# Kernel optimization log

Measured on AMD Instinct MI355X. Metric: run time of the kernel, lower is better.

Reference implementation:

```python
import jax, jax.numpy as jnp
import numpy as np

B = 131072
E = 116            # embedding dim; 12 + E = 128 = layer_sizes[0]
H = 256            # MLP hidden
LATENT = 64

PAIRS = [(0, 1), (0, 2), (1, 2)]
IDS = np.array([[0, 3, 4], [1, 5, 6], [2, 7, 8]])  # ids_in_config, indexed by pair count


def setup_inputs() -> dict:
    key = jax.random.key(0)
    ks = jax.random.split(key, 12)
    d_in = 12 + E  # 128
    s = lambda k, shape, fan_in: jax.random.normal(k, shape, jnp.float32) / np.sqrt(fan_in)
    return {
        "initial_s": jax.random.normal(ks[0], (B, 9), jnp.float32),
        "current_s": jax.random.normal(ks[1], (B, 9), jnp.float32),
        "embeddings": jax.random.normal(ks[2], (B, E), jnp.float32),
        "W1": s(ks[3], (d_in, H), d_in),
        "b1": jnp.zeros((H,), jnp.float32),
        "W2": s(ks[4], (H, H), H),
        "b2": jnp.zeros((H,), jnp.float32),
        "Wm": s(ks[5], (H, LATENT), H),
        "bm": jnp.zeros((LATENT,), jnp.float32),
        "Wv": s(ks[6], (H, LATENT), H),
        "bv": jnp.zeros((LATENT,), jnp.float32),
    }


def _build_inp(initial_s, current_s, embeddings):
    # Replicates the pairwise one-hot + gather + concat construction.
    bsz = initial_s.shape[0]
    eye = jnp.eye(3, dtype=initial_s.dtype)
    feats = []
    for c, (i, j) in enumerate(PAIRS):
        oh = jnp.broadcast_to(jnp.concatenate([eye[i], eye[j]]), (bsz, 6))
        idx = IDS[c]
        feats.append(jnp.concatenate(
            [oh, initial_s[:, idx], current_s[:, idx], embeddings], axis=-1))
    return jnp.stack(feats)  # (3, B, 12+E)


def reference(initial_s, current_s, embeddings, W1, b1, W2, b2, Wm, bm, Wv, bv):
    inp = _build_inp(initial_s, current_s, embeddings)      # (3, B, 128)
    x = jax.nn.relu(jnp.einsum('pbi,ih->pbh', inp, W1) + b1)  # (3, B, 256)
    x = jax.nn.relu(jnp.einsum('pbh,hk->pbk', x, W2) + b2)    # (3, B, 256)
    means = jnp.einsum('pbh,hl->pbl', x, Wm) + bm             # (3, B, 64)
    log_vars = jnp.einsum('pbh,hl->pbl', x, Wv) + bv          # (3, B, 64)
    return (means, log_vars)
```

## Files before the change

kernel.cpp:

```cpp
#include <hip/hip_runtime.h>

typedef __attribute__((ext_vector_type(8))) __bf16 bf16x8;
typedef __attribute__((ext_vector_type(4))) float f32x4;
typedef unsigned int u32;
typedef unsigned long long u64;
typedef unsigned short u16;

#define NB 131072
#define TPB 8

__device__ __forceinline__ u16 f2bf(float f) {
  unsigned int u = __builtin_bit_cast(unsigned int, f);
  u += 0x7fffu + ((u >> 16) & 1u);
  return (u16)(u >> 16);
}

__device__ __forceinline__ u32 cvt_pk(float lo, float hi) {
  u32 r;
  asm("v_cvt_pk_bf16_f32 %0, %1, %2" : "=v"(r) : "v"(lo), "v"(hi));
  return r;
}

#define INP_ADDR(r, byte) (((r) << 8) + ((byte) ^ (((r) & 7) << 4)))
#define X_ADDR(r, byte)   (((r) << 9) + ((byte) ^ (((r) & 7) << 4)))

__global__ void prep_kernel(const float* __restrict__ W1, const float* __restrict__ b1,
                            const float* __restrict__ W2,
                            const float* __restrict__ Wm, const float* __restrict__ Wv,
                            u16* __restrict__ W1f, u16* __restrict__ W2f,
                            u16* __restrict__ Whf, float* __restrict__ b1p) {
  int tid = blockIdx.x * 256 + threadIdx.x;
  int NT = gridDim.x * 256;
  for (int i = tid; i < 32768; i += NT) {
    int j = i & 7, lane = (i >> 3) & 63, f = i >> 9;
    int nf = f & 15, kf = f >> 4;
    int n = nf * 16 + (lane & 15);
    int k = kf * 32 + 8 * (lane >> 4) + j;
    W1f[i] = f2bf(W1[k * 256 + n]);
  }
  for (int i = tid; i < 65536; i += NT) {
    int j = i & 7, lane = (i >> 3) & 63, f = i >> 9;
    int nf = f & 15, kf = f >> 4;
    int n = nf * 16 + (lane & 15);
    int k = kf * 32 + 8 * (lane >> 4) + j;
    W2f[i] = f2bf(W2[k * 256 + n]);
  }
  for (int i = tid; i < 32768; i += NT) {
    int j = i & 7, lane = (i >> 3) & 63, f = i >> 9;
    int nf = f & 7, kf = f >> 3;
    int n = nf * 16 + (lane & 15);
    int k = kf * 32 + 8 * (lane >> 4) + j;
    Whf[i] = f2bf(n < 64 ? Wm[k * 64 + n] : Wv[k * 64 + (n - 64)]);
  }
  if (tid < 768) {
    int p = tid >> 8, h = tid & 255;
    const int r1[3] = {0, 0, 1};
    const int r2[3] = {4, 5, 5};
    b1p[tid] = b1[h] + W1[r1[p] * 256 + h] + W1[r2[p] * 256 + h];
  }
}

__global__ __launch_bounds__(512, 2) void fused_kernel(
    const float* __restrict__ init_s, const float* __restrict__ cur_s,
    const float* __restrict__ emb,
    const u16* __restrict__ W1f, const u16* __restrict__ W2f,
    const u16* __restrict__ Whf,
    const float* __restrict__ b1p, const float* __restrict__ b2,
    const float* __restrict__ bm, const float* __restrict__ bv,
    float* __restrict__ out) {
  extern __shared__ char smem[];
  char* inp = smem;
  char* x1  = smem + 16384;
  char* x2  = smem + 49152;
  char* ost = x1;
  float* sbI = (float*)(smem + 81920);
  float* sbC = (float*)(smem + 81920 + 2304);

  const int t = threadIdx.x;
  const int lane = t & 63;
  const int wave = t >> 6;
  const int ql = lane & 15, qw = lane >> 4;

  bf16x8 w1r[4][2];
#pragma unroll
  for (int kf = 0; kf < 4; ++kf)
#pragma unroll
    for (int ni = 0; ni < 2; ++ni)
      w1r[kf][ni] = *(const bf16x8*)(W1f + (size_t)((kf * 16 + wave * 2 + ni) * 64 + lane) * 8);
  bf16x8 w2r[8][2];
#pragma unroll
  for (int kf = 0; kf < 8; ++kf)
#pragma unroll
    for (int ni = 0; ni < 2; ++ni)
      w2r[kf][ni] = *(const bf16x8*)(W2f + (size_t)((kf * 16 + wave * 2 + ni) * 64 + lane) * 8);
  bf16x8 whr[8];
#pragma unroll
  for (int kf = 0; kf < 8; ++kf)
    whr[kf] = *(const bf16x8*)(Whf + (size_t)((kf * 8 + wave) * 64 + lane) * 8);

  const int hn = wave * 16 + qw * 4;
  const f32x4 hbv = (hn < 64) ? *(const f32x4*)(bm + hn) : *(const f32x4*)(bv + hn - 64);

  if (t < 64) {
    *(u64*)(inp + INP_ADDR(t, 0)) = 0ull;
    *(u32*)(inp + INP_ADDR(t, 8)) = 0u;
  }

  const int IA[3] = {0, 1, 2};
  const int IB[3] = {3, 5, 7};
  const int IC[3] = {4, 6, 8};

#pragma unroll 1
  for (int it = 0; it < TPB; ++it) {
    const int b0 = (blockIdx.x * TPB + it) * 64;

    for (int i = t; i < 64 * 29; i += 512) {
      int r = i / 29;
      int c4 = i - r * 29;
      const f32x4 v = __builtin_nontemporal_load((const f32x4*)(emb + (size_t)(b0 + r) * 116 + c4 * 4));
      u64 pk = (u64)cvt_pk(v[0], v[1]) | ((u64)cvt_pk(v[2], v[3]) << 32);
      *(u64*)(inp + INP_ADDR(r, 24 + 8 * c4)) = pk;
    }
    if (t < 288) {
      int which = t >= 144;
      int idx = which ? t - 144 : t;
      const float* src = which ? cur_s : init_s;
      float* dst = which ? sbC : sbI;
      ((float4*)dst)[idx] = ((const float4*)(src + (size_t)b0 * 9))[idx];
    }

#pragma unroll 1
    for (int p = 0; p < 3; ++p) {
      if (p == 0) __syncthreads();
      if (t < 64) {
        float a0 = sbI[t * 9 + IA[p]], a1 = sbI[t * 9 + IB[p]], a2 = sbI[t * 9 + IC[p]];
        float c0 = sbC[t * 9 + IA[p]], c1 = sbC[t * 9 + IB[p]], c2 = sbC[t * 9 + IC[p]];
        *(u32*)(inp + INP_ADDR(t, 12)) = cvt_pk(a0, a1);
        *(u32*)(inp + INP_ADDR(t, 16)) = cvt_pk(a2, c0);
        *(u32*)(inp + INP_ADDR(t, 20)) = cvt_pk(c1, c2);
      }
      __syncthreads();

      {
        f32x4 acc[4][2];
#pragma unroll
        for (int ni = 0; ni < 2; ++ni) {
          f32x4 bb = *(const f32x4*)(b1p + p * 256 + wave * 32 + ni * 16 + qw * 4);
#pragma unroll
          for (int bf = 0; bf < 4; ++bf) acc[bf][ni] = bb;
        }
#pragma unroll
        for (int kf = 0; kf < 4; ++kf) {
          bf16x8 b[4];
#pragma unroll
          for (int bf = 0; bf < 4; ++bf)
            b[bf] = *(const bf16x8*)(inp + INP_ADDR(bf * 16 + ql, kf * 64 + qw * 16));
#pragma unroll
          for (int ni = 0; ni < 2; ++ni)
#pragma unroll
            for (int bf = 0; bf < 4; ++bf)
              acc[bf][ni] = __builtin_amdgcn_mfma_f32_16x16x32_bf16(w1r[kf][ni], b[bf], acc[bf][ni], 0, 0, 0);
        }
#pragma unroll
        for (int bf = 0; bf < 4; ++bf)
#pragma unroll
          for (int ni = 0; ni < 2; ++ni) {
            f32x4 v = acc[bf][ni];
            u64 pk = (u64)cvt_pk(fmaxf(v[0], 0.f), fmaxf(v[1], 0.f))
                   | ((u64)cvt_pk(fmaxf(v[2], 0.f), fmaxf(v[3], 0.f)) << 32);
            *(u64*)(x1 + X_ADDR(bf * 16 + ql, wave * 64 + ni * 32 + qw * 8)) = pk;
          }
      }
      __syncthreads();

      {
        f32x4 acc[4][2];
#pragma unroll
        for (int ni = 0; ni < 2; ++ni) {
          f32x4 bb = *(const f32x4*)(b2 + wave * 32 + ni * 16 + qw * 4);
#pragma unroll
          for (int bf = 0; bf < 4; ++bf) acc[bf][ni] = bb;
        }
#pragma unroll
        for (int kf = 0; kf < 8; ++kf) {
          bf16x8 b[4];
#pragma unroll
          for (int bf = 0; bf < 4; ++bf)
            b[bf] = *(const bf16x8*)(x1 + X_ADDR(bf * 16 + ql, kf * 64 + qw * 16));
#pragma unroll
          for (int ni = 0; ni < 2; ++ni)
#pragma unroll
            for (int bf = 0; bf < 4; ++bf)
              acc[bf][ni] = __builtin_amdgcn_mfma_f32_16x16x32_bf16(w2r[kf][ni], b[bf], acc[bf][ni], 0, 0, 0);
        }
#pragma unroll
        for (int bf = 0; bf < 4; ++bf)
#pragma unroll
          for (int ni = 0; ni < 2; ++ni) {
            f32x4 v = acc[bf][ni];
            u64 pk = (u64)cvt_pk(fmaxf(v[0], 0.f), fmaxf(v[1], 0.f))
                   | ((u64)cvt_pk(fmaxf(v[2], 0.f), fmaxf(v[3], 0.f)) << 32);
            *(u64*)(x2 + X_ADDR(bf * 16 + ql, wave * 64 + ni * 32 + qw * 8)) = pk;
          }
      }
      __syncthreads();

      {
        f32x4 hacc[4];
#pragma unroll
        for (int bf = 0; bf < 4; ++bf) hacc[bf] = hbv;
#pragma unroll
        for (int kf = 0; kf < 8; ++kf) {
          bf16x8 b[4];
#pragma unroll
          for (int bf = 0; bf < 4; ++bf)
            b[bf] = *(const bf16x8*)(x2 + X_ADDR(bf * 16 + ql, kf * 64 + qw * 16));
#pragma unroll
          for (int bf = 0; bf < 4; ++bf)
            hacc[bf] = __builtin_amdgcn_mfma_f32_16x16x32_bf16(whr[kf], b[bf], hacc[bf], 0, 0, 0);
        }
#pragma unroll
        for (int bf = 0; bf < 4; ++bf) {
          int row = bf * 16 + ql;
          int byte = wave * 64 + qw * 16;
          *(f32x4*)(ost + row * 512 + (byte ^ ((row & 7) << 4))) = hacc[bf];
        }
      }
      __syncthreads();

      for (int i = t; i < 64 * 32; i += 512) {
        int r = i >> 5, c4 = i & 31;
        f32x4 v = *(const f32x4*)(ost + r * 512 + ((c4 * 16) ^ ((r & 7) << 4)));
        size_t off;
        if (c4 < 16)
          off = ((size_t)p * NB + b0 + r) * 64 + (size_t)c4 * 4;
        else
          off = (size_t)3 * NB * 64 + ((size_t)p * NB + b0 + r) * 64 + (size_t)(c4 - 16) * 4;
        __builtin_nontemporal_store(v, (f32x4*)(out + off));
      }
    }
  }
}

extern "C" void kernel_launch(void* const* d_in, const int* in_sizes, int n_in,
                              void* d_out, int out_size, void* d_ws, size_t ws_size,
                              hipStream_t stream) {
  (void)in_sizes; (void)n_in; (void)out_size; (void)ws_size;
  const float* init_s = (const float*)d_in[0];
  const float* cur_s  = (const float*)d_in[1];
  const float* emb    = (const float*)d_in[2];
  const float* W1 = (const float*)d_in[3];
  const float* b1 = (const float*)d_in[4];
  const float* W2 = (const float*)d_in[5];
  const float* b2 = (const float*)d_in[6];
  const float* Wm = (const float*)d_in[7];
  const float* bm = (const float*)d_in[8];
  const float* Wv = (const float*)d_in[9];
  const float* bv = (const float*)d_in[10];

  u16* W1f = (u16*)d_ws;
  u16* W2f = (u16*)((char*)d_ws + 65536);
  u16* Whf = (u16*)((char*)d_ws + 196608);
  float* b1p = (float*)((char*)d_ws + 262144);

  prep_kernel<<<128, 256, 0, stream>>>(W1, b1, W2, Wm, Wv, W1f, W2f, Whf, b1p);

  const int lds_bytes = 16384 + 32768 + 32768 + 4608;
  (void)hipFuncSetAttribute((const void*)fused_kernel,
                            hipFuncAttributeMaxDynamicSharedMemorySize, lds_bytes);
  fused_kernel<<<NB / (64 * TPB), 512, lds_bytes, stream>>>(init_s, cur_s, emb, W1f, W2f, Whf,
                                                            b1p, b2, bm, bv, (float*)d_out);
}
```

Measured before the change: 132.2 us.

## Retile waves as 4 column groups by 2 row halves for MFMA layers

Changes the per-wave work split from 8 waves each owning a narrow column slice across all 64 rows to a 4x2 grid. Each wave now owns 64 output columns over 32 rows. This halves the LDS activation fragment reads per wave per k-step and doubles weight reuse per LDS load. The cost is twice as many weight fragments held in registers per wave (w1r, w2r and whr all double), which raises VGPR pressure and may reduce occupancy or cause spills.

Measured after the change: 304.3 us. 130% more time.

```diff
diff --git a/kernel.cpp b/kernel.cpp
--- a/kernel.cpp
+++ b/kernel.cpp
@@ -79,27 +79,35 @@
   const int t = threadIdx.x;
   const int lane = t & 63;
   const int wave = t >> 6;
+  const int wq = wave & 3;
+  const int rbase = (wave >> 2) * 32;
   const int ql = lane & 15, qw = lane >> 4;
 
-  bf16x8 w1r[4][2];
+  bf16x8 w1r[4][4];
 #pragma unroll
   for (int kf = 0; kf < 4; ++kf)
 #pragma unroll
+    for (int ni = 0; ni < 4; ++ni)
+      w1r[kf][ni] = *(const bf16x8*)(W1f + (size_t)((kf * 16 + wq * 4 + ni) * 64 + lane) * 8);
+  bf16x8 w2r[8][4];
+#pragma unroll
+  for (int kf = 0; kf < 8; ++kf)
+#pragma unroll
+    for (int ni = 0; ni < 4; ++ni)
+      w2r[kf][ni] = *(const bf16x8*)(W2f + (size_t)((kf * 16 + wq * 4 + ni) * 64 + lane) * 8);
+  bf16x8 whr[8][2];
+#pragma unroll
+  for (int kf = 0; kf < 8; ++kf)
+#pragma unroll
     for (int ni = 0; ni < 2; ++ni)
-      w1r[kf][ni] = *(const bf16x8*)(W1f + (size_t)((kf * 16 + wave * 2 + ni) * 64 + lane) * 8);
-  bf16x8 w2r[8][2];
-#pragma unroll
-  for (int kf = 0; kf < 8; ++kf)
-#pragma unroll
-    for (int ni = 0; ni < 2; ++ni)
-      w2r[kf][ni] = *(const bf16x8*)(W2f + (size_t)((kf * 16 + wave * 2 + ni) * 64 + lane) * 8);
-  bf16x8 whr[8];
-#pragma unroll
-  for (int kf = 0; kf < 8; ++kf)
-    whr[kf] = *(const bf16x8*)(Whf + (size_t)((kf * 8 + wave) * 64 + lane) * 8);
-
-  const int hn = wave * 16 + qw * 4;
-  const f32x4 hbv = (hn < 64) ? *(const f32x4*)(bm + hn) : *(const f32x4*)(bv + hn - 64);
+      whr[kf][ni] = *(const bf16x8*)(Whf + (size_t)((kf * 8 + wq * 2 + ni) * 64 + lane) * 8);
+
+  f32x4 hb[2];
+#pragma unroll
+  for (int ni = 0; ni < 2; ++ni) {
+    int hn = wq * 32 + ni * 16 + qw * 4;
+    hb[ni] = (hn < 64) ? *(const f32x4*)(bm + hn) : *(const f32x4*)(bv + hn - 64);
+  }
 
   if (t < 64) {
     *(u64*)(inp + INP_ADDR(t, 0)) = 0ull;
@@ -142,89 +150,95 @@
       __syncthreads();
 
       {
-        f32x4 acc[4][2];
-#pragma unroll
-        for (int ni = 0; ni < 2; ++ni) {
-          f32x4 bb = *(const f32x4*)(b1p + p * 256 + wave * 32 + ni * 16 + qw * 4);
-#pragma unroll
-          for (int bf = 0; bf < 4; ++bf) acc[bf][ni] = bb;
+        f32x4 acc[2][4];
+#pragma unroll
+        for (int ni = 0; ni < 4; ++ni) {
+          f32x4 bb = *(const f32x4*)(b1p + p * 256 + wq * 64 + ni * 16 + qw * 4);
+          acc[0][ni] = bb;
+          acc[1][ni] = bb;
         }
 #pragma unroll
         for (int kf = 0; kf < 4; ++kf) {
-          bf16x8 b[4];
-#pragma unroll
-          for (int bf = 0; bf < 4; ++bf)
-            b[bf] = *(const bf16x8*)(inp + INP_ADDR(bf * 16 + ql, kf * 64 + qw * 16));
-#pragma unroll
-          for (int ni = 0; ni < 2; ++ni)
-#pragma unroll
-            for (int bf = 0; bf < 4; ++bf)
+          bf16x8 b[2];
+#pragma unroll
+          for (int bf = 0; bf < 2; ++bf)
+            b[bf] = *(const bf16x8*)(inp + INP_ADDR(rbase + bf * 16 + ql, kf * 64 + qw * 16));
+#pragma unroll
+          for (int ni = 0; ni < 4; ++ni)
+#pragma unroll
+            for (int bf = 0; bf < 2; ++bf)
               acc[bf][ni] = __builtin_amdgcn_mfma_f32_16x16x32_bf16(w1r[kf][ni], b[bf], acc[bf][ni], 0, 0, 0);
         }
 #pragma unroll
-        for (int bf = 0; bf < 4; ++bf)
-#pragma unroll
-          for (int ni = 0; ni < 2; ++ni) {
+        for (int bf = 0; bf < 2; ++bf)
+#pragma unroll
+          for (int ni = 0; ni < 4; ++ni) {
             f32x4 v = acc[bf][ni];
             u64 pk = (u64)cvt_pk(fmaxf(v[0], 0.f), fmaxf(v[1], 0.f))
                    | ((u64)cvt_pk(fmaxf(v[2], 0.f), fmaxf(v[3], 0.f)) << 32);
-            *(u64*)(x1 + X_ADDR(bf * 16 + ql, wave * 64 + ni * 32 + qw * 8)) = pk;
+            *(u64*)(x1 + X_ADDR(rbase + bf * 16 + ql, wq * 128 + ni * 32 + qw * 8)) = pk;
           }
       }
       __syncthreads();
 
       {
-        f32x4 acc[4][2];
-#pragma unroll
-        for (int ni = 0; ni < 2; ++ni) {
-          f32x4 bb = *(const f32x4*)(b2 + wave * 32 + ni * 16 + qw * 4);
-#pragma unroll
-          for (int bf = 0; bf < 4; ++bf) acc[bf][ni] = bb;
+        f32x4 acc[2][4];
+#pragma unroll
+        for (int ni = 0; ni < 4; ++ni) {
+          f32x4 bb = *(const f32x4*)(b2 + wq * 64 + ni * 16 + qw * 4);
+          acc[0][ni] = bb;
+          acc[1][ni] = bb;
         }
 #pragma unroll
         for (int kf = 0; kf < 8; ++kf) {
-          bf16x8 b[4];
-#pragma unroll
-          for (int bf = 0; bf < 4; ++bf)
-            b[bf] = *(const bf16x8*)(x1 + X_ADDR(bf * 16 + ql, kf * 64 + qw * 16));
-#pragma unroll
-          for (int ni = 0; ni < 2; ++ni)
-#pragma unroll
-            for (int bf = 0; bf < 4; ++bf)
+          bf16x8 b[2];
+#pragma unroll
+          for (int bf = 0; bf < 2; ++bf)
+            b[bf] = *(const bf16x8*)(x1 + X_ADDR(rbase + bf * 16 + ql, kf * 64 + qw * 16));
+#pragma unroll
+          for (int ni = 0; ni < 4; ++ni)
+#pragma unroll
+            for (int bf = 0; bf < 2; ++bf)
               acc[bf][ni] = __builtin_amdgcn_mfma_f32_16x16x32_bf16(w2r[kf][ni], b[bf], acc[bf][ni], 0, 0, 0);
         }
 #pragma unroll
-        for (int bf = 0; bf < 4; ++bf)
-#pragma unroll
-          for (int ni = 0; ni < 2; ++ni) {
+        for (int bf = 0; bf < 2; ++bf)
+#pragma unroll
+          for (int ni = 0; ni < 4; ++ni) {
             f32x4 v = acc[bf][ni];
             u64 pk = (u64)cvt_pk(fmaxf(v[0], 0.f), fmaxf(v[1], 0.f))
                    | ((u64)cvt_pk(fmaxf(v[2], 0.f), fmaxf(v[3], 0.f)) << 32);
-            *(u64*)(x2 + X_ADDR(bf * 16 + ql, wave * 64 + ni * 32 + qw * 8)) = pk;
+            *(u64*)(x2 + X_ADDR(rbase + bf * 16 + ql, wq * 128 + ni * 32 + qw * 8)) = pk;
           }
       }
       __syncthreads();
 
       {
-        f32x4 hacc[4];
-#pragma unroll
-        for (int bf = 0; bf < 4; ++bf) hacc[bf] = hbv;
+        f32x4 hacc[2][2];
+#pragma unroll
+        for (int bf = 0; bf < 2; ++bf)
+#pragma unroll
+          for (int ni = 0; ni < 2; ++ni) hacc[bf][ni] = hb[ni];
 #pragma unroll
         for (int kf = 0; kf < 8; ++kf) {
-          bf16x8 b[4];
-#pragma unroll
-          for (int bf = 0; bf < 4; ++bf)
-            b[bf] = *(const bf16x8*)(x2 + X_ADDR(bf * 16 + ql, kf * 64 + qw * 16));
-#pragma unroll
-          for (int bf = 0; bf < 4; ++bf)
-            hacc[bf] = __builtin_amdgcn_mfma_f32_16x16x32_bf16(whr[kf], b[bf], hacc[bf], 0, 0, 0);
-        }
-#pragma unroll
-        for (int bf = 0; bf < 4; ++bf) {
-          int row = bf * 16 + ql;
-          int byte = wave * 64 + qw * 16;
-          *(f32x4*)(ost + row * 512 + (byte ^ ((row & 7) << 4))) = hacc[bf];
-        }
+          bf16x8 b[2];
+#pragma unroll
+          for (int bf = 0; bf < 2; ++bf)
+            b[bf] = *(const bf16x8*)(x2 + X_ADDR(rbase + bf * 16 + ql, kf * 64 + qw * 16));
+#pragma unroll
+          for (int ni = 0; ni < 2; ++ni)
+#pragma unroll
+            for (int bf = 0; bf < 2; ++bf)
+              hacc[bf][ni] = __builtin_amdgcn_mfma_f32_16x16x32_bf16(whr[kf][ni], b[bf], hacc[bf][ni], 0, 0, 0);
+        }
+#pragma unroll
+        for (int bf = 0; bf < 2; ++bf)
+#pragma unroll
+          for (int ni = 0; ni < 2; ++ni) {
+            int row = rbase + bf * 16 + ql;
+            int byte = wq * 128 + ni * 64 + qw * 16;
+            *(f32x4*)(ost + row * 512 + (byte ^ ((row & 7) << 4))) = hacc[bf][ni];
+          }
       }
       __syncthreads();
 
```

## Software-pipeline MLP stages across steps with fewer barriers and dedicated output buffer

Applied to the files above, without the earlier changes.

Restructures the per-tile loop into a flat step loop. Each step overlaps the export of the previous step's output, the staging of the next inputs and the next layer-1 GEMM with the current layer-2 and head GEMMs. This cuts barriers from about five to two per step. The output stage gets its own LDS region, raising LDS to 112KB. The head GEMM is re-split so all 8 waves work on 32 rows by 32 columns each, and the small state columns are read straight from global memory instead of going through LDS. The larger LDS footprint may cut occupancy from 2 blocks per CU to 1, which could offset the gain from overlap.

New measurement: 137.2 us. 1.04x slower.

```diff
diff --git a/kernel.cpp b/kernel.cpp
--- a/kernel.cpp
+++ b/kernel.cpp
@@ -72,14 +72,14 @@
   char* inp = smem;
   char* x1  = smem + 16384;
   char* x2  = smem + 49152;
-  char* ost = x1;
-  float* sbI = (float*)(smem + 81920);
-  float* sbC = (float*)(smem + 81920 + 2304);
+  char* ost = smem + 81920;
 
   const int t = threadIdx.x;
   const int lane = t & 63;
   const int wave = t >> 6;
   const int ql = lane & 15, qw = lane >> 4;
+  const int rh = wave >> 2;
+  const int hg = wave & 3;
 
   bf16x8 w1r[4][2];
 #pragma unroll
@@ -93,153 +93,173 @@
 #pragma unroll
     for (int ni = 0; ni < 2; ++ni)
       w2r[kf][ni] = *(const bf16x8*)(W2f + (size_t)((kf * 16 + wave * 2 + ni) * 64 + lane) * 8);
-  bf16x8 whr[8];
+  bf16x8 whr[8][2];
 #pragma unroll
   for (int kf = 0; kf < 8; ++kf)
-    whr[kf] = *(const bf16x8*)(Whf + (size_t)((kf * 8 + wave) * 64 + lane) * 8);
-
-  const int hn = wave * 16 + qw * 4;
-  const f32x4 hbv = (hn < 64) ? *(const f32x4*)(bm + hn) : *(const f32x4*)(bv + hn - 64);
+#pragma unroll
+    for (int ni = 0; ni < 2; ++ni)
+      whr[kf][ni] = *(const bf16x8*)(Whf + (size_t)((kf * 8 + hg * 2 + ni) * 64 + lane) * 8);
+
+  f32x4 hb[2];
+#pragma unroll
+  for (int ni = 0; ni < 2; ++ni) {
+    int hn = hg * 32 + ni * 16 + qw * 4;
+    hb[ni] = (hn < 64) ? *(const f32x4*)(bm + hn) : *(const f32x4*)(bv + hn - 64);
+  }
+
+  const int IA[3] = {0, 1, 2};
+  const int IB[3] = {3, 5, 7};
+  const int IC[3] = {4, 6, 8};
+
+  auto stage_emb = [&](int b0n) {
+    for (int i = t; i < 64 * 29; i += 512) {
+      int r = i / 29, c4 = i - r * 29;
+      const f32x4 v = __builtin_nontemporal_load((const f32x4*)(emb + (size_t)(b0n + r) * 116 + c4 * 4));
+      u64 pk = (u64)cvt_pk(v[0], v[1]) | ((u64)cvt_pk(v[2], v[3]) << 32);
+      *(u64*)(inp + INP_ADDR(r, 24 + 8 * c4)) = pk;
+    }
+  };
+  auto stage_scols = [&](int b0n, int np) {
+    if (t < 64) {
+      const float* isr = init_s + (size_t)(b0n + t) * 9;
+      const float* csr = cur_s + (size_t)(b0n + t) * 9;
+      *(u32*)(inp + INP_ADDR(t, 12)) = cvt_pk(isr[IA[np]], isr[IB[np]]);
+      *(u32*)(inp + INP_ADDR(t, 16)) = cvt_pk(isr[IC[np]], csr[IA[np]]);
+      *(u32*)(inp + INP_ADDR(t, 20)) = cvt_pk(csr[IB[np]], csr[IC[np]]);
+    }
+  };
+  auto do_l1 = [&](int s) {
+    const int p1 = s % 3;
+    f32x4 acc[4][2];
+#pragma unroll
+    for (int ni = 0; ni < 2; ++ni) {
+      f32x4 bb = *(const f32x4*)(b1p + p1 * 256 + wave * 32 + ni * 16 + qw * 4);
+#pragma unroll
+      for (int bf = 0; bf < 4; ++bf) acc[bf][ni] = bb;
+    }
+#pragma unroll
+    for (int kf = 0; kf < 4; ++kf) {
+      bf16x8 b[4];
+#pragma unroll
+      for (int bf = 0; bf < 4; ++bf)
+        b[bf] = *(const bf16x8*)(inp + INP_ADDR(bf * 16 + ql, kf * 64 + qw * 16));
+#pragma unroll
+      for (int ni = 0; ni < 2; ++ni)
+#pragma unroll
+        for (int bf = 0; bf < 4; ++bf)
+          acc[bf][ni] = __builtin_amdgcn_mfma_f32_16x16x32_bf16(w1r[kf][ni], b[bf], acc[bf][ni], 0, 0, 0);
+    }
+#pragma unroll
+    for (int bf = 0; bf < 4; ++bf)
+#pragma unroll
+      for (int ni = 0; ni < 2; ++ni) {
+        f32x4 v = acc[bf][ni];
+        u64 pk = (u64)cvt_pk(fmaxf(v[0], 0.f), fmaxf(v[1], 0.f))
+               | ((u64)cvt_pk(fmaxf(v[2], 0.f), fmaxf(v[3], 0.f)) << 32);
+        *(u64*)(x1 + X_ADDR(bf * 16 + ql, wave * 64 + ni * 32 + qw * 8)) = pk;
+      }
+  };
+  auto do_export = [&](int s) {
+    const int pe = s % 3;
+    const int b0e = (blockIdx.x * TPB + s / 3) * 64;
+    for (int i = t; i < 64 * 32; i += 512) {
+      int r = i >> 5, c4 = i & 31;
+      f32x4 v = *(const f32x4*)(ost + r * 512 + ((c4 * 16) ^ ((r & 7) << 4)));
+      size_t off;
+      if (c4 < 16)
+        off = ((size_t)pe * NB + b0e + r) * 64 + (size_t)c4 * 4;
+      else
+        off = (size_t)3 * NB * 64 + ((size_t)pe * NB + b0e + r) * 64 + (size_t)(c4 - 16) * 4;
+      __builtin_nontemporal_store(v, (f32x4*)(out + off));
+    }
+  };
 
   if (t < 64) {
     *(u64*)(inp + INP_ADDR(t, 0)) = 0ull;
     *(u32*)(inp + INP_ADDR(t, 8)) = 0u;
   }
-
-  const int IA[3] = {0, 1, 2};
-  const int IB[3] = {3, 5, 7};
-  const int IC[3] = {4, 6, 8};
+  {
+    const int b00 = blockIdx.x * TPB * 64;
+    stage_emb(b00);
+    stage_scols(b00, 0);
+  }
+  __syncthreads();
+  do_l1(0);
+  __syncthreads();
 
 #pragma unroll 1
-  for (int it = 0; it < TPB; ++it) {
-    const int b0 = (blockIdx.x * TPB + it) * 64;
-
-    for (int i = t; i < 64 * 29; i += 512) {
-      int r = i / 29;
-      int c4 = i - r * 29;
-      const f32x4 v = __builtin_nontemporal_load((const f32x4*)(emb + (size_t)(b0 + r) * 116 + c4 * 4));
-      u64 pk = (u64)cvt_pk(v[0], v[1]) | ((u64)cvt_pk(v[2], v[3]) << 32);
-      *(u64*)(inp + INP_ADDR(r, 24 + 8 * c4)) = pk;
-    }
-    if (t < 288) {
-      int which = t >= 144;
-      int idx = which ? t - 144 : t;
-      const float* src = which ? cur_s : init_s;
-      float* dst = which ? sbC : sbI;
-      ((float4*)dst)[idx] = ((const float4*)(src + (size_t)b0 * 9))[idx];
-    }
-
-#pragma unroll 1
-    for (int p = 0; p < 3; ++p) {
-      if (p == 0) __syncthreads();
-      if (t < 64) {
-        float a0 = sbI[t * 9 + IA[p]], a1 = sbI[t * 9 + IB[p]], a2 = sbI[t * 9 + IC[p]];
-        float c0 = sbC[t * 9 + IA[p]], c1 = sbC[t * 9 + IB[p]], c2 = sbC[t * 9 + IC[p]];
-        *(u32*)(inp + INP_ADDR(t, 12)) = cvt_pk(a0, a1);
-        *(u32*)(inp + INP_ADDR(t, 16)) = cvt_pk(a2, c0);
-        *(u32*)(inp + INP_ADDR(t, 20)) = cvt_pk(c1, c2);
-      }
-      __syncthreads();
-
-      {
-        f32x4 acc[4][2];
+  for (int step = 0; step < 3 * TPB; ++step) {
+    {
+      f32x4 acc[4][2];
+#pragma unroll
+      for (int ni = 0; ni < 2; ++ni) {
+        f32x4 bb = *(const f32x4*)(b2 + wave * 32 + ni * 16 + qw * 4);
+#pragma unroll
+        for (int bf = 0; bf < 4; ++bf) acc[bf][ni] = bb;
+      }
+#pragma unroll
+      for (int kf = 0; kf < 8; ++kf) {
+        bf16x8 b[4];
+#pragma unroll
+        for (int bf = 0; bf < 4; ++bf)
+          b[bf] = *(const bf16x8*)(x1 + X_ADDR(bf * 16 + ql, kf * 64 + qw * 16));
+#pragma unroll
+        for (int ni = 0; ni < 2; ++ni)
+#pragma unroll
+          for (int bf = 0; bf < 4; ++bf)
+            acc[bf][ni] = __builtin_amdgcn_mfma_f32_16x16x32_bf16(w2r[kf][ni], b[bf], acc[bf][ni], 0, 0, 0);
+      }
+      if (step > 0) do_export(step - 1);
+      if (step + 1 < 3 * TPB) {
+        const int s1 = step + 1;
+        const int b0n = (blockIdx.x * TPB + s1 / 3) * 64;
+        if (s1 % 3 == 0) stage_emb(b0n);
+        stage_scols(b0n, s1 % 3);
+      }
+#pragma unroll
+      for (int bf = 0; bf < 4; ++bf)
 #pragma unroll
         for (int ni = 0; ni < 2; ++ni) {
-          f32x4 bb = *(const f32x4*)(b1p + p * 256 + wave * 32 + ni * 16 + qw * 4);
-#pragma unroll
-          for (int bf = 0; bf < 4; ++bf) acc[bf][ni] = bb;
+          f32x4 v = acc[bf][ni];
+          u64 pk = (u64)cvt_pk(fmaxf(v[0], 0.f), fmaxf(v[1], 0.f))
+                 | ((u64)cvt_pk(fmaxf(v[2], 0.f), fmaxf(v[3], 0.f)) << 32);
+          *(u64*)(x2 + X_ADDR(bf * 16 + ql, wave * 64 + ni * 32 + qw * 8)) = pk;
         }
-#pragma unroll
-        for (int kf = 0; kf < 4; ++kf) {
-          bf16x8 b[4];
-#pragma unroll
-          for (int bf = 0; bf < 4; ++bf)
-            b[bf] = *(const bf16x8*)(inp + INP_ADDR(bf * 16 + ql, kf * 64 + qw * 16));
-#pragma unroll
-          for (int ni = 0; ni < 2; ++ni)
-#pragma unroll
-            for (int bf = 0; bf < 4; ++bf)
-              acc[bf][ni] = __builtin_amdgcn_mfma_f32_16x16x32_bf16(w1r[kf][ni], b[bf], acc[bf][ni], 0, 0, 0);
+    }
+    __syncthreads();
+
+    {
+      f32x4 hacc[2][2];
+#pragma unroll
+      for (int bf = 0; bf < 2; ++bf)
+#pragma unroll
+        for (int ni = 0; ni < 2; ++ni) hacc[bf][ni] = hb[ni];
+#pragma unroll
+      for (int kf = 0; kf < 8; ++kf) {
+        bf16x8 b[2];
+#pragma unroll
+        for (int bf = 0; bf < 2; ++bf)
+          b[bf] = *(const bf16x8*)(x2 + X_ADDR(rh * 32 + bf * 16 + ql, kf * 64 + qw * 16));
+#pragma unroll
+        for (int ni = 0; ni < 2; ++ni)
+#pragma unroll
+          for (int bf = 0; bf < 2; ++bf)
+            hacc[bf][ni] = __builtin_amdgcn_mfma_f32_16x16x32_bf16(whr[kf][ni], b[bf], hacc[bf][ni], 0, 0, 0);
+      }
+#pragma unroll
+      for (int bf = 0; bf < 2; ++bf)
+#pragma unroll
+        for (int ni = 0; ni < 2; ++ni) {
+          int row = rh * 32 + bf * 16 + ql;
+          int byte = hg * 128 + ni * 64 + qw * 16;
+          *(f32x4*)(ost + row * 512 + (byte ^ ((row & 7) << 4))) = hacc[bf][ni];
         }
-#pragma unroll
-        for (int bf = 0; bf < 4; ++bf)
-#pragma unroll
-          for (int ni = 0; ni < 2; ++ni) {
-            f32x4 v = acc[bf][ni];
-            u64 pk = (u64)cvt_pk(fmaxf(v[0], 0.f), fmaxf(v[1], 0.f))
-                   | ((u64)cvt_pk(fmaxf(v[2], 0.f), fmaxf(v[3], 0.f)) << 32);
-            *(u64*)(x1 + X_ADDR(bf * 16 + ql, wave * 64 + ni * 32 + qw * 8)) = pk;
-          }
-      }
-      __syncthreads();
-
-      {
-        f32x4 acc[4][2];
-#pragma unroll
-        for (int ni = 0; ni < 2; ++ni) {
-          f32x4 bb = *(const f32x4*)(b2 + wave * 32 + ni * 16 + qw * 4);
-#pragma unroll
-          for (int bf = 0; bf < 4; ++bf) acc[bf][ni] = bb;
-        }
-#pragma unroll
-        for (int kf = 0; kf < 8; ++kf) {
-          bf16x8 b[4];
-#pragma unroll
-          for (int bf = 0; bf < 4; ++bf)
-            b[bf] = *(const bf16x8*)(x1 + X_ADDR(bf * 16 + ql, kf * 64 + qw * 16));
-#pragma unroll
-          for (int ni = 0; ni < 2; ++ni)
-#pragma unroll
-            for (int bf = 0; bf < 4; ++bf)
-              acc[bf][ni] = __builtin_amdgcn_mfma_f32_16x16x32_bf16(w2r[kf][ni], b[bf], acc[bf][ni], 0, 0, 0);
-        }
-#pragma unroll
-        for (int bf = 0; bf < 4; ++bf)
-#pragma unroll
-          for (int ni = 0; ni < 2; ++ni) {
-            f32x4 v = acc[bf][ni];
-            u64 pk = (u64)cvt_pk(fmaxf(v[0], 0.f), fmaxf(v[1], 0.f))
-                   | ((u64)cvt_pk(fmaxf(v[2], 0.f), fmaxf(v[3], 0.f)) << 32);
-            *(u64*)(x2 + X_ADDR(bf * 16 + ql, wave * 64 + ni * 32 + qw * 8)) = pk;
-          }
-      }
-      __syncthreads();
-
-      {
-        f32x4 hacc[4];
-#pragma unroll
-        for (int bf = 0; bf < 4; ++bf) hacc[bf] = hbv;
-#pragma unroll
-        for (int kf = 0; kf < 8; ++kf) {
-          bf16x8 b[4];
-#pragma unroll
-          for (int bf = 0; bf < 4; ++bf)
-            b[bf] = *(const bf16x8*)(x2 + X_ADDR(bf * 16 + ql, kf * 64 + qw * 16));
-#pragma unroll
-          for (int bf = 0; bf < 4; ++bf)
-            hacc[bf] = __builtin_amdgcn_mfma_f32_16x16x32_bf16(whr[kf], b[bf], hacc[bf], 0, 0, 0);
-        }
-#pragma unroll
-        for (int bf = 0; bf < 4; ++bf) {
-          int row = bf * 16 + ql;
-          int byte = wave * 64 + qw * 16;
-          *(f32x4*)(ost + row * 512 + (byte ^ ((row & 7) << 4))) = hacc[bf];
-        }
-      }
-      __syncthreads();
-
-      for (int i = t; i < 64 * 32; i += 512) {
-        int r = i >> 5, c4 = i & 31;
-        f32x4 v = *(const f32x4*)(ost + r * 512 + ((c4 * 16) ^ ((r & 7) << 4)));
-        size_t off;
-        if (c4 < 16)
-          off = ((size_t)p * NB + b0 + r) * 64 + (size_t)c4 * 4;
-        else
-          off = (size_t)3 * NB * 64 + ((size_t)p * NB + b0 + r) * 64 + (size_t)(c4 - 16) * 4;
-        __builtin_nontemporal_store(v, (f32x4*)(out + off));
-      }
-    }
-  }
+      if (step + 1 < 3 * TPB) do_l1(step + 1);
+    }
+    __syncthreads();
+  }
+
+  do_export(3 * TPB - 1);
 }
 
 extern "C" void kernel_launch(void* const* d_in, const int* in_sizes, int n_in,
@@ -265,7 +285,7 @@
 
   prep_kernel<<<128, 256, 0, stream>>>(W1, b1, W2, Wm, Wv, W1f, W2f, Whf, b1p);
 
-  const int lds_bytes = 16384 + 32768 + 32768 + 4608;
+  const int lds_bytes = 16384 + 32768 + 32768 + 32768;
   (void)hipFuncSetAttribute((const void*)fused_kernel,
                             hipFuncAttributeMaxDynamicSharedMemorySize, lds_bytes);
   fused_kernel<<<NB / (64 * TPB), 512, lds_bytes, stream>>>(init_s, cur_s, emb, W1f, W2f, Whf,
```
